# Performance work log

Hardware: AMD Instinct MI355X
Metric: run time of the kernel (lower is better)

## Reference

```python
import jax, jax.numpy as jnp
import numpy as np


def setup_inputs() -> dict:
    key = jax.random.key(0)
    ks = jax.random.split(key, 3)
    B, d_in, d_latent = 8192, 768, 12288
    x = jax.random.normal(ks[0], (B, d_in), dtype=jnp.float32)
    # kaiming_normal fan_in relu: std = sqrt(2/d_in)
    W_enc = jax.random.normal(ks[1], (d_latent, d_in), dtype=jnp.float32) * np.sqrt(2.0 / d_in)
    b_enc = jnp.zeros((d_latent,), dtype=jnp.float32)
    # xavier_normal: std = sqrt(2/(d_in+d_latent))
    W_dec = jax.random.normal(ks[2], (d_in, d_latent), dtype=jnp.float32) * np.sqrt(2.0 / (d_in + d_latent))
    b_dec = jnp.zeros((d_in,), dtype=jnp.float32)
    b_pre = jnp.zeros((d_in,), dtype=jnp.float32)
    return {"x": x, "b_pre": b_pre, "W_enc": W_enc, "b_enc": b_enc,
            "W_dec": W_dec, "b_dec": b_dec, "k": 64}


def reference(x, b_pre, W_enc, b_enc, W_dec, b_dec, k):
    # encode: a = (x - b_pre) @ W_enc.T + b_enc   -> (B, d_latent)
    x0 = x - b_pre
    a = jnp.einsum('bi,li->bl', x0, W_enc) + b_enc
    # topk activation (mode='value', nonneg=True): relu then keep k largest
    a_relu = jax.nn.relu(a)
    topk_val, topk_idx = jax.lax.top_k(a_relu, k)  # (B, k)
    B = a.shape[0]
    rows = jnp.arange(B)[:, None]
    z = jnp.zeros_like(a).at[rows, topk_idx].set(topk_val)
    # decode: x_hat = z @ W_dec.T + b_dec
    x_hat = jnp.einsum('bl,il->bi', z, W_dec) + b_dec
    return (x_hat, z, a)
```

## Files before the change

kernel.cpp:

```cpp
#include <hip/hip_runtime.h>

#define DIN 768
#define DL  12288
#define CAP 320
#define MARGIN 0.03f
#define UB 0.015f
#define UMAX 64
#define KMAX 128

typedef __attribute__((ext_vector_type(8))) _Float16 half8;
typedef __attribute__((ext_vector_type(4))) _Float16 half4v;
typedef __attribute__((ext_vector_type(4))) float f32x4;

__device__ __forceinline__ void gl_lds16(const void* g, void* s) {
  __builtin_amdgcn_global_load_lds(
      (const __attribute__((address_space(1))) unsigned int*)g,
      (__attribute__((address_space(3))) unsigned int*)s, 16, 0, 0);
}
__device__ __forceinline__ void wait_lgkm0_fence() {
  asm volatile("s_waitcnt lgkmcnt(0)" ::: "memory");
  __builtin_amdgcn_sched_barrier(0);
}
__device__ __forceinline__ void wait_vm0() {
  asm volatile("s_waitcnt vmcnt(0)" ::: "memory");
}

#define NBX (8192 * DIN / 1024)
#define NBW (DL * DIN / 1024)
#define NBT ((DL / 32) * (DIN / 32))

__global__ __launch_bounds__(256) void k_prep(
    const float* __restrict__ x, const float* __restrict__ b_pre,
    const float* __restrict__ W_enc, const float* __restrict__ W_dec,
    _Float16* __restrict__ Ah, _Float16* __restrict__ Bh, _Float16* __restrict__ WT)
{
  const int b = blockIdx.x, tid = threadIdx.x;
  if (b < NBX) {
    const int i4 = b * 256 + tid;
    const int col4 = (i4 % (DIN / 4)) * 4;
    const float4 xv = *(const float4*)&x[(size_t)i4 * 4];
    const float4 bp = *(const float4*)&b_pre[col4];
    half4v o;
    o.x = (_Float16)(xv.x - bp.x);
    o.y = (_Float16)(xv.y - bp.y);
    o.z = (_Float16)(xv.z - bp.z);
    o.w = (_Float16)(xv.w - bp.w);
    *(half4v*)&Ah[(size_t)i4 * 4] = o;
  } else if (b < NBX + NBW) {
    const int i4 = (b - NBX) * 256 + tid;
    const float4 wv = *(const float4*)&W_enc[(size_t)i4 * 4];
    half4v o;
    o.x = (_Float16)wv.x; o.y = (_Float16)wv.y;
    o.z = (_Float16)wv.z; o.w = (_Float16)wv.w;
    *(half4v*)&Bh[(size_t)i4 * 4] = o;
  } else {
    const int idx = b - NBX - NBW;
    const int c0 = (idx % (DL / 32)) * 32;
    const int r0 = (idx / (DL / 32)) * 32;
    const int xx = tid & 31, yy = tid >> 5;
    __shared__ float t[32][33];
#pragma unroll
    for (int dy = 0; dy < 32; dy += 8)
      t[yy + dy][xx] = W_dec[(size_t)(r0 + yy + dy) * DL + c0 + xx];
    __syncthreads();
#pragma unroll
    for (int dy = 0; dy < 32; dy += 8)
      WT[(size_t)(c0 + yy + dy) * DIN + r0 + xx] = (_Float16)t[xx][yy + dy];
  }
}

#define BM 256
#define BN 256
#define BKE 64
#define NKT (DIN / BKE)

__global__ __launch_bounds__(512) void k_encode_f16(
    const _Float16* __restrict__ Ah, const _Float16* __restrict__ Bh,
    const float* __restrict__ b_enc, float* __restrict__ aout)
{
  __shared__ _Float16 sA[2][BM][BKE];
  __shared__ _Float16 sB[2][BN][BKE];
  const int tid = threadIdx.x, wave = tid >> 6, lane = tid & 63;
  const int wm = wave >> 2, wn = wave & 3;
  const int fr = lane & 15, fc = lane >> 4;

  const int q = ((8192 / BM) * (DL / BN)) >> 3;
  const int wg = (blockIdx.x & 7) * q + (blockIdx.x >> 3);
  const int bm = (wg / (DL / BN)) * BM;
  const int bn = (wg % (DL / BN)) * BN;

  const int lrow = lane >> 3;
  const int lcol = ((lane & 7) ^ lrow) << 3;
  const _Float16* gA = Ah + (size_t)(bm + lrow) * DIN + lcol;
  const _Float16* gB = Bh + (size_t)(bn + lrow) * DIN + lcol;

  f32x4 acc[8][4];
#pragma unroll
  for (int i = 0; i < 8; ++i)
#pragma unroll
    for (int j = 0; j < 4; ++j) acc[i][j] = f32x4{0.f, 0.f, 0.f, 0.f};

#define STAGE_TILE(buf, tt)                                                      \
  {                                                                              \
    _Pragma("unroll")                                                            \
    for (int s4 = 0; s4 < 4; ++s4) {                                             \
      const int s8 = (wave + s4 * 8) * 8;                                        \
      gl_lds16(gA + (size_t)s8 * DIN + (tt) * BKE, &sA[buf][s8][0]);             \
      gl_lds16(gB + (size_t)s8 * DIN + (tt) * BKE, &sB[buf][s8][0]);             \
    }                                                                            \
  }

#define LOADQ(p, mh, nh)                                                         \
  {                                                                              \
    const char* bA = (const char*)&sA[p][0][0];                                  \
    const char* bB = (const char*)&sB[p][0][0];                                  \
    _Pragma("unroll")                                                            \
    for (int i = 0; i < 4; ++i)                                                  \
      _Pragma("unroll")                                                          \
      for (int ks = 0; ks < 2; ++ks) {                                           \
        const int row = wm * 128 + ((mh) * 4 + i) * 16 + fr;                     \
        const int ph = (ks * 4 + fc) ^ (fr & 7);                                 \
        af[i][ks] = *(const half8*)(bA + row * (BKE * 2) + ph * 16);             \
      }                                                                          \
    _Pragma("unroll")                                                            \
    for (int j = 0; j < 2; ++j)                                                  \
      _Pragma("unroll")                                                          \
      for (int ks = 0; ks < 2; ++ks) {                                           \
        const int row = wn * 64 + ((nh) * 2 + j) * 16 + fr;                      \
        const int ph = (ks * 4 + fc) ^ (fr & 7);                                 \
        bf[j][ks] = *(const half8*)(bB + row * (BKE * 2) + ph * 16);             \
      }                                                                          \
  }

#define MFMAQ(mh, nh)                                                            \
  __builtin_amdgcn_s_setprio(1);                                                 \
  _Pragma("unroll")                                                              \
  for (int i = 0; i < 4; ++i)                                                    \
    _Pragma("unroll")                                                            \
    for (int j = 0; j < 2; ++j)                                                  \
      _Pragma("unroll")                                                          \
      for (int ks = 0; ks < 2; ++ks)                                             \
        acc[(mh) * 4 + i][(nh) * 2 + j] = __builtin_amdgcn_mfma_f32_16x16x32_f16( \
            af[i][ks], bf[j][ks], acc[(mh) * 4 + i][(nh) * 2 + j], 0, 0, 0);     \
  __builtin_amdgcn_s_setprio(0);

  half8 af[4][2], bf[2][2];

  STAGE_TILE(0, 0)
  wait_vm0();
  __builtin_amdgcn_s_barrier();

#pragma unroll 1
  for (int t = 0; t < NKT; ++t) {
    const int p = t & 1;
    LOADQ(p, 0, 0)
    if (t + 1 < NKT) STAGE_TILE(p ^ 1, t + 1)
    __builtin_amdgcn_s_barrier();
    wait_lgkm0_fence();
    MFMAQ(0, 0)
    __builtin_amdgcn_s_barrier();
    LOADQ(p, 0, 1)
    __builtin_amdgcn_s_barrier();
    wait_lgkm0_fence();
    MFMAQ(0, 1)
    __builtin_amdgcn_s_barrier();
    LOADQ(p, 1, 0)
    __builtin_amdgcn_s_barrier();
    wait_lgkm0_fence();
    MFMAQ(1, 0)
    __builtin_amdgcn_s_barrier();
    LOADQ(p, 1, 1)
    wait_vm0();
    __builtin_amdgcn_s_barrier();
    wait_lgkm0_fence();
    MFMAQ(1, 1)
    __builtin_amdgcn_s_barrier();
  }

#pragma unroll
  for (int j = 0; j < 4; ++j) {
    const int col = bn + wn * 64 + j * 16 + fr;
    const float be = b_enc[col];
#pragma unroll
    for (int i = 0; i < 8; ++i) {
      const int row0 = bm + wm * 128 + i * 16 + fc * 4;
#pragma unroll
      for (int r = 0; r < 4; ++r)
        aout[(size_t)(row0 + r) * DL + col] = acc[i][j][r] + be;
    }
  }
#undef STAGE_TILE
#undef LOADQ
#undef MFMAQ
}

template <int ZERO_Z>
__global__ __launch_bounds__(512) void k_fused(
    const float* __restrict__ a, const float* __restrict__ x,
    const float* __restrict__ b_pre, const float* __restrict__ W,
    const float* __restrict__ b_enc, const int* __restrict__ kp,
    const _Float16* __restrict__ WT, const float* __restrict__ b_dec,
    float* __restrict__ z, float* __restrict__ xhat)
{
  const int row = blockIdx.x, tid = threadIdx.x;
  const int wave = tid >> 6, lane = tid & 63;
  const int kk = min(max(kp[0], 1), KMAX);
  const float* ar = a + (size_t)row * DL;
  float* zr = z + (size_t)row * DL;

  __shared__ unsigned hist[4][512];
  __shared__ float s_wmax[8];
  __shared__ unsigned s_wsuf[8];
  __shared__ float s_Tm;
  __shared__ int s_cnt;
  __shared__ int cidx[CAP];
  __shared__ float caf[CAP];
  __shared__ double x0[DIN];
  __shared__ float s_ak;
  __shared__ int s_ucnt, s_nw;
  __shared__ int uidx[UMAX];
  __shared__ double uex[UMAX];
  __shared__ int widx[KMAX];
  __shared__ float wval[KMAX];

  float4 v[6];
#pragma unroll
  for (int j = 0; j < 6; ++j) {
    float4 t4 = ((const float4*)ar)[tid + 512 * j];
    t4.x = fmaxf(t4.x, 0.f); t4.y = fmaxf(t4.y, 0.f);
    t4.z = fmaxf(t4.z, 0.f); t4.w = fmaxf(t4.w, 0.f);
    v[j] = t4;
    if (ZERO_Z) {
      const float4 zz = {0.f, 0.f, 0.f, 0.f};
      ((float4*)zr)[tid + 512 * j] = zz;
    }
  }
  for (int i = tid; i < DIN; i += 512)
    x0[i] = (double)x[(size_t)row * DIN + i] - (double)b_pre[i];
  float m = 0.f;
#pragma unroll
  for (int j = 0; j < 6; ++j)
    m = fmaxf(m, fmaxf(fmaxf(v[j].x, v[j].y), fmaxf(v[j].z, v[j].w)));
#pragma unroll
  for (int off = 32; off; off >>= 1) m = fmaxf(m, __shfl_xor(m, off));
  if (lane == 0) s_wmax[wave] = m;
  if (tid == 0) { s_cnt = 0; s_Tm = -1.f; s_ak = -1e30f; s_ucnt = 0; s_nw = 0; }
  __syncthreads();
  float rmax = s_wmax[0];
#pragma unroll
  for (int w2 = 1; w2 < 8; ++w2) rmax = fmaxf(rmax, s_wmax[w2]);

  float Tm;
  if (rmax <= 0.f) {
    Tm = 1e30f;
  } else {
    const float scale = 512.f / rmax;
    unsigned need = (unsigned)kk;
    bool found = false;
    for (int phase = 0; phase < 2 && !found; ++phase) {
      for (int i = tid; i < 4 * 512; i += 512) (&hist[0][0])[i] = 0u;
      __syncthreads();
      unsigned* h = hist[wave & 3];
      const float sc = (phase == 0) ? scale : scale * 8.f;
#pragma unroll
      for (int j = 0; j < 6; ++j) {
        const float vv[4] = {v[j].x, v[j].y, v[j].z, v[j].w};
#pragma unroll
        for (int e = 0; e < 4; ++e) {
          const float val = vv[e];
          if (val > 0.f) {
            const float fb = val * scale;
            if (phase == 0) {
              if (fb >= 64.f) atomicAdd(&h[min(511, (int)fb)], 1u);
            } else {
              if (fb < 64.f) atomicAdd(&h[min(511, (int)(val * sc))], 1u);
            }
          }
        }
      }
      __syncthreads();
      const unsigned st = hist[0][tid] + hist[1][tid] + hist[2][tid] + hist[3][tid];
      unsigned s = st;
#pragma unroll
      for (int off = 1; off < 64; off <<= 1) {
        const unsigned o = __shfl_down(s, off);
        if (lane + off < 64) s += o;
      }
      if (lane == 0) s_wsuf[wave] = s;
      __syncthreads();
      unsigned above_w = 0, total = 0;
#pragma unroll
      for (int w2 = 0; w2 < 8; ++w2) {
        total += s_wsuf[w2];
        if (w2 > wave) above_w += s_wsuf[w2];
      }
      const unsigned inc = s + above_w;
      const unsigned excl = inc - st;
      if (total >= need) {
        if (inc >= need && excl < need)
          s_Tm = (float)tid / sc - MARGIN;
        found = true;
      } else {
        need -= total;
      }
      __syncthreads();
    }
    Tm = s_Tm;
  }

#pragma unroll
  for (int j = 0; j < 6; ++j) {
    const float vv[4] = {v[j].x, v[j].y, v[j].z, v[j].w};
#pragma unroll
    for (int e = 0; e < 4; ++e) {
      if (vv[e] > 0.f && vv[e] >= Tm) {
        const int p = atomicAdd(&s_cnt, 1);
        if (p < CAP) { cidx[p] = (tid + 512 * j) * 4 + e; caf[p] = vv[e]; }
      }
    }
  }
  __syncthreads();
  const int C = min(s_cnt, CAP);

  if (C > kk) {
    if (tid < C) {
      const float mv = caf[tid];
      const int mi = cidx[tid];
      int r = 0;
      for (int j = 0; j < C; ++j) {
        const float fj = caf[j];
        if (fj > mv || (fj == mv && cidx[j] < mi)) ++r;
      }
      if (r == kk - 1) s_ak = mv;
    }
    __syncthreads();
  }
  const float ak = s_ak;

  if (tid < C) {
    const float mv = caf[tid];
    if (C <= kk || mv > ak + UB) {
      const int p = atomicAdd(&s_nw, 1);
      widx[p] = cidx[tid]; wval[p] = mv;
    } else if (mv >= ak - UB) {
      const int p = atomicAdd(&s_ucnt, 1);
      if (p < UMAX) uidx[p] = cidx[tid];
    }
  }
  __syncthreads();
  const int ci = s_nw;
  const int ucnt = min(s_ucnt, UMAX);

  for (int c = wave; c < ucnt; c += 8) {
    const int idx = uidx[c];
    const float* wrow = W + (size_t)idx * DIN;
    double s = 0.0;
#pragma unroll
    for (int it = 0; it < DIN / 64; ++it)
      s = fma(x0[lane + it * 64], (double)wrow[lane + it * 64], s);
#pragma unroll
    for (int mm = 32; mm; mm >>= 1) s += __shfl_xor(s, mm);
    if (lane == 0) {
      const double e = s + (double)b_enc[idx];
      uex[c] = e > 0.0 ? e : 0.0;
    }
  }
  __syncthreads();

  const int utake = min(kk - ci, ucnt);
  if (tid < ucnt) {
    const double mv = uex[tid];
    const int mi = uidx[tid];
    int r = 0;
    for (int j = 0; j < ucnt; ++j) {
      const double fj = uex[j];
      if (fj > mv || (fj == mv && uidx[j] < mi)) ++r;
    }
    if (r < utake) {
      const int p = atomicAdd(&s_nw, 1);
      widx[p] = mi; wval[p] = (float)mv;
    }
  }
  __syncthreads();
  const int nW = s_nw;

  if (tid < nW) zr[widx[tid]] = wval[tid];

  if (tid < 192) {
    float4 acc = ((const float4*)b_dec)[tid];
    for (int j = 0; j < nW; ++j) {
      const float vv = wval[j];
      const half4v w4 = *(const half4v*)(WT + (size_t)widx[j] * DIN + tid * 4);
      acc.x = fmaf(vv, (float)w4.x, acc.x);
      acc.y = fmaf(vv, (float)w4.y, acc.y);
      acc.z = fmaf(vv, (float)w4.z, acc.z);
      acc.w = fmaf(vv, (float)w4.w, acc.w);
    }
    ((float4*)(xhat + (size_t)row * DIN))[tid] = acc;
  }
}

extern "C" void kernel_launch(void* const* d_in, const int* in_sizes, int n_in,
                              void* d_out, int out_size, void* d_ws, size_t ws_size,
                              hipStream_t stream)
{
  const float* x     = (const float*)d_in[0];
  const float* b_pre = (const float*)d_in[1];
  const float* W_enc = (const float*)d_in[2];
  const float* b_enc = (const float*)d_in[3];
  const float* W_dec = (const float*)d_in[4];
  const float* b_dec = (const float*)d_in[5];
  const int*   kp    = (const int*)d_in[6];
  const int M = in_sizes[0] / DIN;

  float* xhat = (float*)d_out;
  float* z    = xhat + (size_t)M * DIN;
  float* a    = z + (size_t)M * DL;

  const bool bigws = ws_size >= ((size_t)192 << 20);
  _Float16 *WT16, *Ah, *Bh;
  if (bigws) {
    WT16 = (_Float16*)((char*)d_ws + ((size_t)1 << 20));
    Ah   = (_Float16*)((char*)d_ws + ((size_t)64 << 20));
    Bh   = (_Float16*)((char*)d_ws + ((size_t)96 << 20));
  } else {
    WT16 = (_Float16*)z;
    Ah   = (_Float16*)(z + (size_t)12 * 1024 * 1024);
    Bh   = (_Float16*)(z + (size_t)20 * 1024 * 1024);
  }

  if (bigws) {
    hipMemsetAsync(z, 0, (size_t)M * DL * sizeof(float), stream);
    k_prep<<<NBX + NBW + NBT, 256, 0, stream>>>(x, b_pre, W_enc, W_dec, Ah, Bh, WT16);
    k_encode_f16<<<(M / BM) * (DL / BN), 512, 0, stream>>>(Ah, Bh, b_enc, a);
    k_fused<0><<<M, 512, 0, stream>>>(a, x, b_pre, W_enc, b_enc, kp, WT16, b_dec, z, xhat);
  } else {
    k_prep<<<NBX + NBW + NBT, 256, 0, stream>>>(x, b_pre, W_enc, W_dec, Ah, Bh, WT16);
    k_encode_f16<<<(M / BM) * (DL / BN), 512, 0, stream>>>(Ah, Bh, b_enc, a);
    k_fused<1><<<M, 512, 0, stream>>>(a, x, b_pre, W_enc, b_enc, kp, WT16, b_dec, z, xhat);
  }
}
```

Before: 687.4 us.

## Emit top-k candidates above fixed threshold in encoder epilogue, skip full row scan

The encoder GEMM epilogue now atomically appends, per row, every activation above a fixed threshold (2.9) into a candidate buffer. A new fast kernel runs top-k on that short list, zeroes z inline instead of a separate full memset, and does the decode. Rows with too few or too many candidates, or whose k-th value sits near the threshold, are flagged, and only those are reprocessed by the original full-row kernel. The fixed threshold is tuned to the activation distribution of the test inputs, and the global atomics in the GEMM epilogue add contention.

```diff
diff --git a/kernel.cpp b/kernel.cpp
--- a/kernel.cpp
+++ b/kernel.cpp
@@ -3,6 +3,8 @@
 #define DIN 768
 #define DL  12288
 #define CAP 320
+#define CAP2 512
+#define TCAND 2.9f
 #define MARGIN 0.03f
 #define UB 0.015f
 #define UMAX 64
@@ -74,9 +76,11 @@
 #define BKE 64
 #define NKT (DIN / BKE)
 
+template <int EMIT>
 __global__ __launch_bounds__(512) void k_encode_f16(
     const _Float16* __restrict__ Ah, const _Float16* __restrict__ Bh,
-    const float* __restrict__ b_enc, float* __restrict__ aout)
+    const float* __restrict__ b_enc, float* __restrict__ aout,
+    int* __restrict__ cnt, int2* __restrict__ cand)
 {
   __shared__ _Float16 sA[2][BM][BKE];
   __shared__ _Float16 sB[2][BN][BKE];
@@ -185,8 +189,17 @@
     for (int i = 0; i < 8; ++i) {
       const int row0 = bm + wm * 128 + i * 16 + fc * 4;
 #pragma unroll
-      for (int r = 0; r < 4; ++r)
-        aout[(size_t)(row0 + r) * DL + col] = acc[i][j][r] + be;
+      for (int r = 0; r < 4; ++r) {
+        const float v = acc[i][j][r] + be;
+        aout[(size_t)(row0 + r) * DL + col] = v;
+        if (EMIT && v > TCAND) {
+          const int p2 = atomicAdd(&cnt[row0 + r], 1);
+          if (p2 < CAP2) {
+            int2 pk; pk.x = __float_as_int(v); pk.y = col;
+            cand[(size_t)(row0 + r) * CAP2 + p2] = pk;
+          }
+        }
+      }
     }
   }
 #undef STAGE_TILE
@@ -194,15 +207,141 @@
 #undef MFMAQ
 }
 
-template <int ZERO_Z>
-__global__ __launch_bounds__(512) void k_fused(
+__global__ __launch_bounds__(512) void k_fast(
+    const int* __restrict__ cnt, const int2* __restrict__ cand,
+    const float* __restrict__ x, const float* __restrict__ b_pre,
+    const float* __restrict__ W, const float* __restrict__ b_enc,
+    const int* __restrict__ kp, const _Float16* __restrict__ WT,
+    const float* __restrict__ b_dec, float* __restrict__ z,
+    float* __restrict__ xhat, int* __restrict__ flag)
+{
+  const int row = blockIdx.x, tid = threadIdx.x;
+  const int wave = tid >> 6, lane = tid & 63;
+  const int kk = min(max(kp[0], 1), KMAX);
+  float* zr = z + (size_t)row * DL;
+
+  __shared__ float cv[CAP2];
+  __shared__ int ci[CAP2];
+  __shared__ double x0[DIN];
+  __shared__ float s_ak;
+  __shared__ int s_nw, s_ucnt;
+  __shared__ int uidx[UMAX];
+  __shared__ double uex[UMAX];
+  __shared__ int widx[KMAX];
+  __shared__ float wval[KMAX];
+
+  const float4 zz = {0.f, 0.f, 0.f, 0.f};
+#pragma unroll
+  for (int j = 0; j < 6; ++j) ((float4*)zr)[tid + 512 * j] = zz;
+
+  const int Craw = cnt[row];
+  const int C = min(Craw, CAP2);
+  for (int i = tid; i < C; i += 512) {
+    const int2 p = cand[(size_t)row * CAP2 + i];
+    cv[i] = __int_as_float(p.x);
+    ci[i] = p.y;
+  }
+  for (int i = tid; i < DIN; i += 512)
+    x0[i] = (double)x[(size_t)row * DIN + i] - (double)b_pre[i];
+  if (tid == 0) { s_ak = -1e30f; s_nw = 0; s_ucnt = 0; }
+  __syncthreads();
+
+  bool defic = (Craw >= CAP2) || (C < kk);
+  if (!defic) {
+    if (tid < C) {
+      const float mv = cv[tid];
+      const int mi = ci[tid];
+      int r = 0;
+      for (int j = 0; j < C; ++j) {
+        const float fj = cv[j];
+        if (fj > mv || (fj == mv && ci[j] < mi)) ++r;
+      }
+      if (r == kk - 1) s_ak = mv;
+    }
+    __syncthreads();
+    if (s_ak - UB <= TCAND) defic = true;
+  } else {
+    __syncthreads();
+  }
+  if (defic) {
+    if (tid == 0) flag[row] = 1;
+    return;
+  }
+  const float ak = s_ak;
+
+  if (tid < C) {
+    const float mv = cv[tid];
+    if (mv > ak + UB) {
+      const int p = atomicAdd(&s_nw, 1);
+      widx[p] = ci[tid]; wval[p] = mv;
+    } else if (mv >= ak - UB) {
+      const int p = atomicAdd(&s_ucnt, 1);
+      if (p < UMAX) uidx[p] = ci[tid];
+    }
+  }
+  __syncthreads();
+  const int nci = s_nw;
+  const int ucnt = min(s_ucnt, UMAX);
+
+  for (int c = wave; c < ucnt; c += 8) {
+    const int idx = uidx[c];
+    const float* wrow = W + (size_t)idx * DIN;
+    double s = 0.0;
+#pragma unroll
+    for (int it = 0; it < DIN / 64; ++it)
+      s = fma(x0[lane + it * 64], (double)wrow[lane + it * 64], s);
+#pragma unroll
+    for (int mm = 32; mm; mm >>= 1) s += __shfl_xor(s, mm);
+    if (lane == 0) {
+      const double e = s + (double)b_enc[idx];
+      uex[c] = e > 0.0 ? e : 0.0;
+    }
+  }
+  __syncthreads();
+
+  const int utake = min(kk - nci, ucnt);
+  if (tid < ucnt) {
+    const double mv = uex[tid];
+    const int mi = uidx[tid];
+    int r = 0;
+    for (int j = 0; j < ucnt; ++j) {
+      const double fj = uex[j];
+      if (fj > mv || (fj == mv && uidx[j] < mi)) ++r;
+    }
+    if (r < utake) {
+      const int p = atomicAdd(&s_nw, 1);
+      widx[p] = mi; wval[p] = (float)mv;
+    }
+  }
+  __syncthreads();
+  const int nW = s_nw;
+
+  if (tid < nW) zr[widx[tid]] = wval[tid];
+
+  if (tid < 192) {
+    float4 acc = ((const float4*)b_dec)[tid];
+    for (int j = 0; j < nW; ++j) {
+      const float vv = wval[j];
+      const half4v w4 = *(const half4v*)(WT + (size_t)widx[j] * DIN + tid * 4);
+      acc.x = fmaf(vv, (float)w4.x, acc.x);
+      acc.y = fmaf(vv, (float)w4.y, acc.y);
+      acc.z = fmaf(vv, (float)w4.z, acc.z);
+      acc.w = fmaf(vv, (float)w4.w, acc.w);
+    }
+    ((float4*)(xhat + (size_t)row * DIN))[tid] = acc;
+  }
+}
+
+template <int FORCE_ALL, int ZERO_Z>
+__global__ __launch_bounds__(512) void k_full(
     const float* __restrict__ a, const float* __restrict__ x,
     const float* __restrict__ b_pre, const float* __restrict__ W,
     const float* __restrict__ b_enc, const int* __restrict__ kp,
     const _Float16* __restrict__ WT, const float* __restrict__ b_dec,
-    float* __restrict__ z, float* __restrict__ xhat)
+    float* __restrict__ z, float* __restrict__ xhat, const int* __restrict__ flag)
 {
   const int row = blockIdx.x, tid = threadIdx.x;
+  if (!FORCE_ALL && flag[row] == 0) return;
   const int wave = tid >> 6, lane = tid & 63;
   const int kk = min(max(kp[0], 1), KMAX);
   const float* ar = a + (size_t)row * DL;
@@ -348,7 +487,7 @@
     }
   }
   __syncthreads();
-  const int ci = s_nw;
+  const int nci = s_nw;
   const int ucnt = min(s_ucnt, UMAX);
 
   for (int c = wave; c < ucnt; c += 8) {
@@ -367,7 +506,7 @@
   }
   __syncthreads();
 
-  const int utake = min(kk - ci, ucnt);
+  const int utake = min(kk - nci, ucnt);
   if (tid < ucnt) {
     const double mv = uex[tid];
     const int mi = uidx[tid];
@@ -418,25 +557,31 @@
   float* a    = z + (size_t)M * DL;
 
   const bool bigws = ws_size >= ((size_t)192 << 20);
-  _Float16 *WT16, *Ah, *Bh;
+
   if (bigws) {
-    WT16 = (_Float16*)((char*)d_ws + ((size_t)1 << 20));
-    Ah   = (_Float16*)((char*)d_ws + ((size_t)64 << 20));
-    Bh   = (_Float16*)((char*)d_ws + ((size_t)96 << 20));
+    int*      cnt  = (int*)d_ws;
+    int*      flag = (int*)d_ws + M;
+    int2*     cand = (int2*)((char*)d_ws + ((size_t)1 << 20));
+    _Float16* WT16 = (_Float16*)((char*)d_ws + ((size_t)40 << 20));
+    _Float16* Ah   = (_Float16*)((char*)d_ws + ((size_t)64 << 20));
+    _Float16* Bh   = (_Float16*)((char*)d_ws + ((size_t)96 << 20));
+
+    hipMemsetAsync(d_ws, 0, 2 * M * sizeof(int), stream);
+    k_prep<<<NBX + NBW + NBT, 256, 0, stream>>>(x, b_pre, W_enc, W_dec, Ah, Bh, WT16);
+    k_encode_f16<1><<<(M / BM) * (DL / BN), 512, 0, stream>>>(Ah, Bh, b_enc, a, cnt, cand);
+    k_fast<<<M, 512, 0, stream>>>(cnt, cand, x, b_pre, W_enc, b_enc, kp, WT16, b_dec,
+                                  z, xhat, flag);
+    k_full<0, 0><<<M, 512, 0, stream>>>(a, x, b_pre, W_enc, b_enc, kp, WT16, b_dec,
+                                        z, xhat, flag);
   } else {
-    WT16 = (_Float16*)z;
-    Ah   = (_Float16*)(z + (size_t)12 * 1024 * 1024);
-    Bh   = (_Float16*)(z + (size_t)20 * 1024 * 1024);
-  }
-
-  if (bigws) {
-    hipMemsetAsync(z, 0, (size_t)M * DL * sizeof(float), stream);
+    _Float16* WT16 = (_Float16*)z;
+    _Float16* Ah   = (_Float16*)(z + (size_t)12 * 1024 * 1024);
+    _Float16* Bh   = (_Float16*)(z + (size_t)20 * 1024 * 1024);
+
     k_prep<<<NBX + NBW + NBT, 256, 0, stream>>>(x, b_pre, W_enc, W_dec, Ah, Bh, WT16);
-    k_encode_f16<<<(M / BM) * (DL / BN), 512, 0, stream>>>(Ah, Bh, b_enc, a);
-    k_fused<0><<<M, 512, 0, stream>>>(a, x, b_pre, W_enc, b_enc, kp, WT16, b_dec, z, xhat);
-  } else {
-    k_prep<<<NBX + NBW + NBT, 256, 0, stream>>>(x, b_pre, W_enc, W_dec, Ah, Bh, WT16);
-    k_encode_f16<<<(M / BM) * (DL / BN), 512, 0, stream>>>(Ah, Bh, b_enc, a);
-    k_fused<1><<<M, 512, 0, stream>>>(a, x, b_pre, W_enc, b_enc, kp, WT16, b_dec, z, xhat);
-  }
-}
+    k_encode_f16<0><<<(M / BM) * (DL / BN), 512, 0, stream>>>(Ah, Bh, b_enc, a,
+                                                              nullptr, nullptr);
+    k_full<1, 1><<<M, 512, 0, stream>>>(a, x, b_pre, W_enc, b_enc, kp, WT16, b_dec,
+                                        z, xhat, nullptr);
+  }
+}
```

After: 1.029 ms. 49.8% more time.
